# Optimization experiments

Hardware: AMD Instinct MI355X
Metric: run time of the kernel (lower is better)

The kernel has to match this reference:

```python
import jax, jax.numpy as jnp
import numpy as np

SIGMA = 1.0  # gaussian kernel bandwidth (init arg)
AE = 1.0     # affinity scale (default forward arg)


def setup_inputs() -> dict:
    key = jax.random.key(0)
    k1, k2, k3, k4 = jax.random.split(key, 4)
    b, n, d, input_dim = 2, 8192, 1, 64
    return {
        "Xs": jax.random.normal(k1, (b, n, d), dtype=jnp.float32),
        "Ys": jax.random.normal(k2, (b, n, d), dtype=jnp.float32),
        "Ws": jax.random.normal(k3, (b, input_dim), dtype=jnp.float32),
        "A_w": jax.random.normal(k4, (d, input_dim), dtype=jnp.float32) * 0.1,
        "A_b": jnp.zeros((d,), dtype=jnp.float32),
    }


def reference(Xs, Ys, Ws, A_w, A_b):
    # Xs, Ys: (b, N, 1) edgewise scalar features; Ws: (b, input_dim) global weights.
    # use_global=True: gate X by tanh(Linear(W)) -> scalar coefficient per graph (d=1).
    coef = jnp.tanh(Ws @ A_w.T + A_b)          # (b, 1)
    X = Xs[..., 0] * coef                       # (b, N) scaled features
    Y = Ys[..., 0]                              # (b, N)
    # pairwise squared L2 over the (size-1) feature dim -> (b, N, N)
    dist = (X[:, :, None] - Y[:, None, :]) ** 2
    dist = jnp.where(jnp.isnan(dist), jnp.inf, dist)  # NaN -> Inf mask
    Me = jnp.exp(-dist / SIGMA) * AE
    return Me
```

## Files before the change

### kernel.cpp

```cpp
#include <hip/hip_runtime.h>

__global__ void coef_kernel(const float* __restrict__ Ws,
                            const float* __restrict__ A_w,
                            const float* __restrict__ A_b,
                            float* __restrict__ coef,
                            int b, int input_dim) {
    int bi = blockIdx.x * blockDim.x + threadIdx.x;
    if (bi < b) {
        float acc = A_b[0];
        const float* w = Ws + (size_t)bi * input_dim;
        for (int k = 0; k < input_dim; ++k) acc += w[k] * A_w[k];
        coef[bi] = tanhf(acc);
    }
}

__global__ void __launch_bounds__(256)
me_kernel(const float* __restrict__ Xs,
          const float* __restrict__ Ys,
          const float* __restrict__ coef,
          float* __restrict__ out,
          int N) {
    const int row  = blockIdx.x;
    const int bIdx = row / N;
    const float xi = Xs[row] * coef[bIdx];

    const float4* __restrict__ Y4 = reinterpret_cast<const float4*>(Ys + (size_t)bIdx * N);
    float4* __restrict__ O4 = reinterpret_cast<float4*>(out + (size_t)row * N);
    const int nvec = N >> 2;

    for (int v = threadIdx.x; v < nvec; v += blockDim.x) {
        float4 y = Y4[v];
        float dx = xi - y.x;
        float dy = xi - y.y;
        float dz = xi - y.z;
        float dw = xi - y.w;
        float4 o;
        o.x = __expf(-(dx * dx));
        o.y = __expf(-(dy * dy));
        o.z = __expf(-(dz * dz));
        o.w = __expf(-(dw * dw));
        O4[v] = o;
    }
}

extern "C" void kernel_launch(void* const* d_in, const int* in_sizes, int n_in,
                              void* d_out, int out_size, void* d_ws, size_t ws_size,
                              hipStream_t stream) {
    const float* Xs  = (const float*)d_in[0];
    const float* Ys  = (const float*)d_in[1];
    const float* Ws  = (const float*)d_in[2];
    const float* A_w = (const float*)d_in[3];
    const float* A_b = (const float*)d_in[4];
    float* out = (float*)d_out;

    const int d         = in_sizes[4];
    const int input_dim = in_sizes[3] / d;
    const int b         = in_sizes[2] / input_dim;
    const int N         = in_sizes[0] / (b * d);

    float* coef = (float*)d_ws;

    coef_kernel<<<1, 64, 0, stream>>>(Ws, A_w, A_b, coef, b, input_dim);
    me_kernel<<<b * N, 256, 0, stream>>>(Xs, Ys, coef, out, N);
}
```

Before: 107.2 us.

## Fuse coef computation into main kernel, process four rows per block, nontemporal stores

Removes the separate coef kernel launch by having every block recompute the tanh-gated linear coefficient from Ws and A_w. Each block now handles four output rows, reusing each loaded Y vector four times and cutting the grid size by four. Output writes use nontemporal stores to avoid polluting the cache with the large write-once output. The trade-offs are that the 64-element dot product is recomputed in every block and the kernel assumes N is divisible by four.

After: 88.90 us. 17.1% less time.

```diff
diff --git a/kernel.cpp b/kernel.cpp
--- a/kernel.cpp
+++ b/kernel.cpp
@@ -1,45 +1,66 @@
 #include <hip/hip_runtime.h>
 
-__global__ void coef_kernel(const float* __restrict__ Ws,
-                            const float* __restrict__ A_w,
-                            const float* __restrict__ A_b,
-                            float* __restrict__ coef,
-                            int b, int input_dim) {
-    int bi = blockIdx.x * blockDim.x + threadIdx.x;
-    if (bi < b) {
-        float acc = A_b[0];
-        const float* w = Ws + (size_t)bi * input_dim;
-        for (int k = 0; k < input_dim; ++k) acc += w[k] * A_w[k];
-        coef[bi] = tanhf(acc);
-    }
-}
+typedef float f32x4 __attribute__((ext_vector_type(4)));
 
 __global__ void __launch_bounds__(256)
 me_kernel(const float* __restrict__ Xs,
           const float* __restrict__ Ys,
-          const float* __restrict__ coef,
+          const float* __restrict__ Ws,
+          const float* __restrict__ A_w,
+          const float* __restrict__ A_b,
           float* __restrict__ out,
-          int N) {
-    const int row  = blockIdx.x;
-    const int bIdx = row / N;
-    const float xi = Xs[row] * coef[bIdx];
+          int N, int input_dim) {
+    const int ROWS = 4;
+    const int blocksPerBatch = N / ROWS;
+    const int bIdx = blockIdx.x / blocksPerBatch;
+    const int r0   = blockIdx.x * ROWS;
 
-    const float4* __restrict__ Y4 = reinterpret_cast<const float4*>(Ys + (size_t)bIdx * N);
-    float4* __restrict__ O4 = reinterpret_cast<float4*>(out + (size_t)row * N);
+    float acc = A_b[0];
+    const float* __restrict__ w = Ws + (size_t)bIdx * input_dim;
+    #pragma unroll 16
+    for (int k = 0; k < input_dim; ++k) acc += w[k] * A_w[k];
+    const float coef = tanhf(acc);
+
+    const float x0 = Xs[r0 + 0] * coef;
+    const float x1 = Xs[r0 + 1] * coef;
+    const float x2 = Xs[r0 + 2] * coef;
+    const float x3 = Xs[r0 + 3] * coef;
+
+    const f32x4* __restrict__ Y4 = reinterpret_cast<const f32x4*>(Ys + (size_t)bIdx * N);
+    f32x4* __restrict__ O0 = reinterpret_cast<f32x4*>(out + (size_t)(r0 + 0) * N);
+    f32x4* __restrict__ O1 = reinterpret_cast<f32x4*>(out + (size_t)(r0 + 1) * N);
+    f32x4* __restrict__ O2 = reinterpret_cast<f32x4*>(out + (size_t)(r0 + 2) * N);
+    f32x4* __restrict__ O3 = reinterpret_cast<f32x4*>(out + (size_t)(r0 + 3) * N);
+
     const int nvec = N >> 2;
 
-    for (int v = threadIdx.x; v < nvec; v += blockDim.x) {
-        float4 y = Y4[v];
-        float dx = xi - y.x;
-        float dy = xi - y.y;
-        float dz = xi - y.z;
-        float dw = xi - y.w;
-        float4 o;
-        o.x = __expf(-(dx * dx));
-        o.y = __expf(-(dy * dy));
-        o.z = __expf(-(dz * dz));
-        o.w = __expf(-(dw * dw));
-        O4[v] = o;
+    for (int v = threadIdx.x; v < nvec; v += 256) {
+        const f32x4 y = Y4[v];
+        f32x4 o0, o1, o2, o3;
+        {
+            float a = x0 - y.x, b2 = x0 - y.y, c = x0 - y.z, e = x0 - y.w;
+            o0.x = __expf(-(a * a)); o0.y = __expf(-(b2 * b2));
+            o0.z = __expf(-(c * c)); o0.w = __expf(-(e * e));
+        }
+        {
+            float a = x1 - y.x, b2 = x1 - y.y, c = x1 - y.z, e = x1 - y.w;
+            o1.x = __expf(-(a * a)); o1.y = __expf(-(b2 * b2));
+            o1.z = __expf(-(c * c)); o1.w = __expf(-(e * e));
+        }
+        {
+            float a = x2 - y.x, b2 = x2 - y.y, c = x2 - y.z, e = x2 - y.w;
+            o2.x = __expf(-(a * a)); o2.y = __expf(-(b2 * b2));
+            o2.z = __expf(-(c * c)); o2.w = __expf(-(e * e));
+        }
+        {
+            float a = x3 - y.x, b2 = x3 - y.y, c = x3 - y.z, e = x3 - y.w;
+            o3.x = __expf(-(a * a)); o3.y = __expf(-(b2 * b2));
+            o3.z = __expf(-(c * c)); o3.w = __expf(-(e * e));
+        }
+        __builtin_nontemporal_store(o0, &O0[v]);
+        __builtin_nontemporal_store(o1, &O1[v]);
+        __builtin_nontemporal_store(o2, &O2[v]);
+        __builtin_nontemporal_store(o3, &O3[v]);
     }
 }
 
@@ -58,8 +79,6 @@
     const int b         = in_sizes[2] / input_dim;
     const int N         = in_sizes[0] / (b * d);
 
-    float* coef = (float*)d_ws;
-
-    coef_kernel<<<1, 64, 0, stream>>>(Ws, A_w, A_b, coef, b, input_dim);
-    me_kernel<<<b * N, 256, 0, stream>>>(Xs, Ys, coef, out, N);
+    const int ROWS = 4;
+    me_kernel<<<(b * N) / ROWS, 256, 0, stream>>>(Xs, Ys, Ws, A_w, A_b, out, N, input_dim);
 }
```
